# Kernel tuning notes

Hardware: AMD Instinct MI355X
Metric: run time of the kernel (lower is better)

## Reference

```python
import jax, jax.numpy as jnp
import numpy as np

EPS = 1e-8
FS = 10000
WIN_LEN = 256          # N_FRAME
HOP = WIN_LEN // 2     # 128
NFFT = 2 * WIN_LEN     # 512
NUMBAND = 15
MINFREQ = 150
N_INTEL = 30           # N, number of frames per intelligibility segment
BETA = -15.0
DYN_RANGE = 40.0


def _thirdoct(fs, nfft, num_bands, min_freq):
    """One-third octave band matrix (pystoi.utils.thirdoct)."""
    f = np.linspace(0, fs, nfft + 1)[: nfft // 2 + 1]
    k = np.arange(num_bands, dtype=np.float64)
    freq_low = min_freq * np.power(2.0, (2 * k - 1) / 6)
    freq_high = min_freq * np.power(2.0, (2 * k + 1) / 6)
    obm = np.zeros((num_bands, len(f)), dtype=np.float32)
    for i in range(num_bands):
        fl = int(np.argmin(np.square(f - freq_low[i])))
        fh = int(np.argmin(np.square(f - freq_high[i])))
        obm[i, fl:fh] = 1.0
    return obm


def _frame(x, framelen, hop):
    """x: (B, T) -> (B, nf, framelen) sliding frames (static index gather)."""
    T = x.shape[-1]
    nf = (T - framelen) // hop + 1
    idx = np.arange(framelen)[None, :] + hop * np.arange(nf)[:, None]
    return x[:, idx]


def _stoi(est, tgt, win, obm):
    B = tgt.shape[0]
    # ---- VAD: remove silent frames (stable-partition kept frames to front) ----
    xf = _frame(tgt, WIN_LEN, HOP) * win           # (B, nf, L)
    yf = _frame(est, WIN_LEN, HOP) * win
    energies = 20.0 * jnp.log10(jnp.linalg.norm(xf, axis=-1) + EPS)  # (B, nf)
    mask = (energies.max(-1, keepdims=True) - DYN_RANGE - energies) < 0
    nf = xf.shape[1]
    # stable argsort: kept (mask=True -> key 0) frames first, original order preserved
    order = jnp.argsort(jnp.logical_not(mask).astype(jnp.int32), axis=-1)
    xf = jnp.take_along_axis(xf, order[..., None], axis=1)
    yf = jnp.take_along_axis(yf, order[..., None], axis=1)
    counts = mask.sum(-1)                          # (B,) number of kept frames
    keep = (jnp.arange(nf)[None, :] < counts[:, None]).astype(xf.dtype)
    xf = xf * keep[..., None]
    yf = yf * keep[..., None]

    # ---- overlap-and-add (framelen == 2 * hop) -> (B, (nf+1)*HOP) ----
    def ola(fr):
        a = fr[:, :, :HOP].reshape(B, -1)
        b = fr[:, :, HOP:].reshape(B, -1)
        return jnp.pad(a, ((0, 0), (0, HOP))) + jnp.pad(b, ((0, 0), (HOP, 0)))

    x_sil = ola(xf)
    y_sil = ola(yf)

    # mask sorted descending then first element dropped -> ones at positions < count-1
    m = (jnp.arange(nf - 1)[None, :] < (counts[:, None] - 1)).astype(xf.dtype)  # (B, nf-1)

    # ---- STFT via framing + rfft (last frame dropped, as in module) ----
    def stft(x):
        fr = _frame(x, WIN_LEN, HOP)[:, :-1] * win        # (B, nf-1, L)
        return jnp.fft.rfft(fr, n=NFFT, axis=-1)          # (B, nf-1, F)

    x_spec = stft(x_sil) * m[..., None]
    y_spec = stft(y_sil) * m[..., None]

    # ---- one-third octave band energies ----
    x_tob = jnp.sqrt(jnp.einsum('kf,bnf->bkn', obm, jnp.abs(x_spec) ** 2) + EPS)
    y_tob = jnp.sqrt(jnp.einsum('kf,bnf->bkn', obm, jnp.abs(y_spec) ** 2) + EPS)

    # ---- N_INTEL-frame segments (unfold) ----
    n_stft = x_tob.shape[-1]
    M = n_stft - N_INTEL + 1
    sidx = np.arange(N_INTEL)[:, None] + np.arange(M)[None, :]
    x_seg = x_tob[:, :, sidx]                      # (B, K, N, M)
    y_seg = y_tob[:, :, sidx]
    m2 = m[:, N_INTEL - 1:]                        # (B, M)
    x_seg = x_seg * m2[:, None, None, :]
    y_seg = y_seg * m2[:, None, None, :]

    # ---- clipped, normalized correlation (non-extended STOI) ----
    norm_const = jnp.linalg.norm(x_seg, axis=2, keepdims=True) / (
        jnp.linalg.norm(y_seg, axis=2, keepdims=True) + EPS)
    clip_val = 10.0 ** (-BETA / 20.0)
    y_prim = jnp.minimum(y_seg * norm_const, x_seg * (1.0 + clip_val))
    y_prim = y_prim - y_prim.mean(2, keepdims=True)
    x_c = x_seg - x_seg.mean(2, keepdims=True)
    y_prim = y_prim / (jnp.linalg.norm(y_prim, axis=2, keepdims=True) + EPS)
    x_c = x_c / (jnp.linalg.norm(x_c, axis=2, keepdims=True) + EPS)
    corr = (y_prim * x_c).sum(2).mean(1)           # (B, M)
    out = corr.sum(-1) / (m2.sum(-1) + EPS)        # (B,)
    return -out


def setup_inputs() -> dict:
    key = jax.random.key(0)
    k1, k2 = jax.random.split(key)
    B, T = 32, 320000
    targets = jax.random.normal(k1, (B, T), dtype=jnp.float32)
    est_targets = targets + 0.3 * jax.random.normal(k2, (B, T), dtype=jnp.float32)
    win = jnp.asarray(np.hanning(WIN_LEN + 2)[1:-1], dtype=jnp.float32)
    obm = jnp.asarray(_thirdoct(FS, NFFT, NUMBAND, MINFREQ))
    return {"est_targets": est_targets, "targets": targets, "win": win, "obm": obm}


def reference(est_targets, targets, win, obm):
    return _stoi(est_targets, targets, win, obm)
```

## Files before the change

### kernel.cpp

```cpp
#include <hip/hip_runtime.h>
#include <math.h>

#define EPSF 1e-8f
#define WIN_LEN 256
#define HOP 128
#define NBINS 257
#define NUMBAND 15
#define NFRAMES 2499
#define NSTFT 2498
#define N_INTEL 30
#define NSEG 2469
#define NB 32
#define T_LEN 320000
#define CLIP_VAL 5.623413251903491f
#define NHALF 2500
#define AB_STRIDE 2560

typedef float v2f __attribute__((ext_vector_type(2)));
typedef float v4f __attribute__((ext_vector_type(4)));

__device__ __forceinline__ void pk_fma_blo(v2f& d, v2f a, v2f b) {
    asm("v_pk_fma_f32 %0, %1, %2, %0 op_sel:[0,0,0] op_sel_hi:[1,0,1]"
        : "+v"(d) : "v"(a), "v"(b));
}
__device__ __forceinline__ void pk_fma_bhi(v2f& d, v2f a, v2f b) {
    asm("v_pk_fma_f32 %0, %1, %2, %0 op_sel:[0,1,0] op_sel_hi:[1,1,1]"
        : "+v"(d) : "v"(a), "v"(b));
}
__device__ __forceinline__ void pk_fma_rot(v2f& d, v2f a, v2f b) {
    asm("v_pk_fma_f32 %0, %1, %2, %0 op_sel:[1,1,0] op_sel_hi:[0,1,1] neg_lo:[1,0,0]"
        : "+v"(d) : "v"(a), "v"(b));
}
__device__ __forceinline__ void pk_rot(v2f& cs, v2f cksk) {
    v2f t;
    asm("v_pk_mul_f32 %0, %1, %2 op_sel:[0,0] op_sel_hi:[1,0]"
        : "=v"(t) : "v"(cs), "v"(cksk));
    asm("v_pk_fma_f32 %0, %0, %1, %2 op_sel:[1,1,0] op_sel_hi:[0,1,1] neg_lo:[1,0,0]"
        : "+v"(cs) : "v"(cksk), "v"(t));
}
__device__ __forceinline__ v2f pk_cmul(v2f a, v2f b) {
    v2f t;
    asm("v_pk_mul_f32 %0, %1, %2 op_sel:[0,0] op_sel_hi:[1,0]"
        : "=v"(t) : "v"(a), "v"(b));
    asm("v_pk_fma_f32 %0, %1, %2, %0 op_sel:[1,1,0] op_sel_hi:[0,1,1] neg_lo:[1,0,0]"
        : "+v"(t) : "v"(a), "v"(b));
    return t;
}

#define WS_COUNTS   0
#define WS_BANDLO   512
#define WS_BANDHI   768
#define WS_ACC      1024
#define WS_SRCFRM   2048
#define WS_XTOB     324096
#define WS_YTOB     5120512

__global__ __launch_bounds__(256)
void k1a_ab(const float* __restrict__ tgt, const float* __restrict__ win,
            float2* __restrict__ ab)
{
    const int b = blockIdx.x;
    const int h = blockIdx.y * 256 + threadIdx.x;
    if (h >= NHALF) return;
    const float* xp = tgt + (size_t)b * T_LEN + (size_t)h * HOP;
    float sa = 0.f, sb = 0.f;
    #pragma unroll 4
    for (int u = 0; u < HOP; u += 4) {
        const float4 xv = *(const float4*)(xp + u);
        const float4 wl = *(const float4*)(win + u);
        const float4 wh = *(const float4*)(win + HOP + u);
        float a;
        a = xv.x * wl.x; sa = fmaf(a, a, sa);
        a = xv.y * wl.y; sa = fmaf(a, a, sa);
        a = xv.z * wl.z; sa = fmaf(a, a, sa);
        a = xv.w * wl.w; sa = fmaf(a, a, sa);
        a = xv.x * wh.x; sb = fmaf(a, a, sb);
        a = xv.y * wh.y; sb = fmaf(a, a, sb);
        a = xv.z * wh.z; sb = fmaf(a, a, sb);
        a = xv.w * wh.w; sb = fmaf(a, a, sb);
    }
    ab[(size_t)b * AB_STRIDE + h] = make_float2(sa, sb);
}

__global__ __launch_bounds__(256)
void k1b_scan(const float2* __restrict__ ab, const float* __restrict__ obm,
              int* __restrict__ counts, int* __restrict__ srcfrm,
              int* __restrict__ band_lo, int* __restrict__ band_hi,
              float* __restrict__ acc)
{
    const int b = blockIdx.x;
    const int tid = threadIdx.x;
    __shared__ float nr[NFRAMES];
    __shared__ float red[256];
    __shared__ int   sc[256];

    const float2* abp = ab + (size_t)b * AB_STRIDE;
    for (int f = tid; f < NFRAMES; f += 256) {
        const float2 p0 = abp[f];
        const float2 p1 = abp[f + 1];
        nr[f] = sqrtf(p0.x + p1.y);
    }
    __syncthreads();

    float mx = 0.f;
    for (int f = tid; f < NFRAMES; f += 256) mx = fmaxf(mx, nr[f]);
    red[tid] = mx;
    __syncthreads();
    for (int s = 128; s > 0; s >>= 1) {
        if (tid < s) red[tid] = fmaxf(red[tid], red[tid + s]);
        __syncthreads();
    }
    const float thr = (red[0] + EPSF) * 0.01f;

    const int c0 = tid * 10;
    const int c1 = (c0 + 10 < NFRAMES) ? c0 + 10 : NFRAMES;
    int lc = 0;
    for (int f = c0; f < c1; ++f) if (nr[f] + EPSF > thr) ++lc;
    sc[tid] = lc;
    __syncthreads();
    #pragma unroll
    for (int off = 1; off < 256; off <<= 1) {
        int u = (tid >= off) ? sc[tid - off] : 0;
        __syncthreads();
        sc[tid] += u;
        __syncthreads();
    }
    if (tid == 0) {
        counts[b] = sc[255];
        acc[b] = 0.f;
    }
    int pos = sc[tid] - lc;
    int* sf = srcfrm + b * NFRAMES;
    for (int f = c0; f < c1; ++f) if (nr[f] + EPSF > thr) sf[pos++] = f;

    if (b == 0 && tid < NUMBAND) {
        int lo = -1, hi = 0;
        for (int k = 0; k < NBINS; ++k) {
            if (obm[tid * NBINS + k] != 0.f) { if (lo < 0) lo = k; hi = k + 1; }
        }
        band_lo[tid] = (lo < 0) ? 0 : lo;
        band_hi[tid] = hi;
    }
    __syncthreads();
    if (b == 0 && tid == 0) {
        int lo = NBINS, hi = 0;
        for (int i = 0; i < NUMBAND; ++i) {
            if (band_lo[i] < lo) lo = band_lo[i];
            if (band_hi[i] > hi) hi = band_hi[i];
        }
        band_lo[NUMBAND] = lo;
        band_hi[NUMBAND] = hi;
    }
}

__global__ __launch_bounds__(128)
void k2_stft_tob(const float* __restrict__ est, const float* __restrict__ tgt,
                 const float* __restrict__ win,
                 const int* __restrict__ counts, const int* __restrict__ srcfrm,
                 const int* __restrict__ band_lo, const int* __restrict__ band_hi,
                 float* __restrict__ xtob, float* __restrict__ ytob)
{
    const int lin = blockIdx.x;
    const int xcd = lin & 7, cidx = lin >> 3;
    const int q = NSTFT >> 3, r = NSTFT & 7;
    const int j = (xcd < r ? xcd * (q + 1) : r * (q + 1) + (xcd - r) * q) + cidx;

    const int b = blockIdx.y;
    const int cntb = counts[b];
    if (j >= cntb - 1) return;

    const int tid = threadIdx.x;
    __shared__ v4f   sxy[512];
    __shared__ float frf[512];

    const int* sf = srcfrm + b * NFRAMES;
    const float* xg = tgt + (size_t)b * T_LEN;
    const float* yg = est + (size_t)b * T_LEN;

    {
        const int t2 = 2 * tid;
        const int k0 = sf[j];
        const v2f wa = *(const v2f*)&win[t2];
        v2f xv, yv;
        if (tid < 64) {
            xv = *(const v2f*)&xg[k0 * HOP + t2] * wa;
            yv = *(const v2f*)&yg[k0 * HOP + t2] * wa;
            if (j >= 1) {
                const int km = sf[j - 1];
                const v2f wb = *(const v2f*)&win[HOP + t2];
                xv += *(const v2f*)&xg[km * HOP + HOP + t2] * wb;
                yv += *(const v2f*)&yg[km * HOP + HOP + t2] * wb;
            }
        } else {
            const int kp = sf[j + 1];
            const v2f wb = *(const v2f*)&win[t2 - HOP];
            xv = *(const v2f*)&xg[k0 * HOP + t2] * wa
               + *(const v2f*)&xg[kp * HOP + t2 - HOP] * wb;
            yv = *(const v2f*)&yg[k0 * HOP + t2] * wa
               + *(const v2f*)&yg[kp * HOP + t2 - HOP] * wb;
        }
        const v4f st = { xv.x * wa.x, yv.x * wa.x, xv.y * wa.y, yv.y * wa.y };
        *(v4f*)&frf[4 * tid] = st;
    }
    __syncthreads();

    {
        const int m = tid & 7;
        const int c = tid >> 3;
        const float ang = -0.19634954084936207f * (float)m;
        const v2f cksk = { __cosf(ang), __sinf(ang) };
        v2f cs = { 1.f, 0.f };
        v2f Tx0 = {0,0}, Tx1 = {0,0}, Tx2 = {0,0}, Tx3 = {0,0};
        v2f Ty0 = {0,0}, Ty1 = {0,0}, Ty2 = {0,0}, Ty3 = {0,0};
        #pragma unroll
        for (int t1 = 0; t1 < 16; ++t1) {
            const v2f va = *(const v2f*)&frf[2 * (t1 * 16 + c)];
            if ((t1 & 3) == 0)      { pk_fma_blo(Tx0, cs, va); pk_fma_bhi(Ty0, cs, va); }
            else if ((t1 & 3) == 1) { pk_fma_blo(Tx1, cs, va); pk_fma_bhi(Ty1, cs, va); }
            else if ((t1 & 3) == 2) { pk_fma_blo(Tx2, cs, va); pk_fma_bhi(Ty2, cs, va); }
            else                    { pk_fma_blo(Tx3, cs, va); pk_fma_bhi(Ty3, cs, va); }
            pk_rot(cs, cksk);
        }
        const v2f Ax = Tx0 + Tx2, Bx = Tx0 - Tx2, Cx = Tx1 + Tx3, Dx = Tx1 - Tx3;
        const v2f Ay = Ty0 + Ty2, By = Ty0 - Ty2, Cy = Ty1 + Ty3, Dy = Ty1 - Ty3;
        const v2f S0x = Ax + Cx, S2x = Ax - Cx;
        const v2f S0y = Ay + Cy, S2y = Ay - Cy;
        const v2f S1x = { Bx.x + Dx.y, Bx.y - Dx.x };
        const v2f S1y = { By.x + Dy.y, By.y - Dy.x };
        const v2f S3x = { Bx.x - Dx.y, Bx.y + Dx.x };
        const v2f S3y = { By.x - Dy.y, By.y + Dy.x };
        sxy[c * 32 + m]      = (v4f){ S0x.x, S0x.y, S0y.x, S0y.y };
        sxy[c * 32 + m + 8]  = (v4f){ S1x.x, S1x.y, S1y.x, S1y.y };
        sxy[c * 32 + m + 16] = (v4f){ S2x.x, S2x.y, S2y.x, S2y.y };
        sxy[c * 32 + m + 24] = (v4f){ S3x.x, S3x.y, S3y.x, S3y.y };
    }
    __syncthreads();

    const int blo = band_lo[NUMBAND];
    const int bhi = band_hi[NUMBAND];
    (void)bhi;
    const int base = blo & ~31;
    float* px = frf;
    float* py = frf + 224;
    if (tid < 64) {
        const int m2 = tid & 31;
        const int sig = tid >> 5;
        const int sbyte = m2 * 16 + sig * 8;
        const float ang = -0.012271846303085130f * (float)(base + m2);
        const v2f cksk = { __cosf(ang), __sinf(ang) };
        v2f cs = { 1.f, 0.f };
        v2f V[16];
        #pragma unroll
        for (int t0 = 0; t0 < 16; ++t0) {
            const v2f s = *(const v2f*)((const char*)sxy + (t0 * 512 + sbyte));
            V[t0] = (t0 == 0) ? s : pk_cmul(cs, s);
            pk_rot(cs, cksk);
        }
        v2f G[4][4];
        #pragma unroll
        for (int rr = 0; rr < 4; ++rr) {
            const v2f A = V[rr] + V[rr + 8];
            const v2f B = V[rr] - V[rr + 8];
            const v2f C = V[rr + 4] + V[rr + 12];
            const v2f D = V[rr + 4] - V[rr + 12];
            G[0][rr] = A + C;
            G[2][rr] = A - C;
            G[1][rr] = (v2f){ B.x + D.y, B.y - D.x };
            G[3][rr] = (v2f){ B.x - D.y, B.y + D.x };
        }
        float* pout = sig ? py : px;
        #define C1 0.92387953251f
        #define S1 0.38268343236f
        #define C2 0.70710678119f
        #define XOUT(P, D, W1R, W1I, W2R, W2I, W3R, W3I) { \
            float xr_ = G[D][0].x, xi_ = G[D][0].y; \
            xr_ += (W1R)*G[D][1].x - (W1I)*G[D][1].y; xi_ += (W1R)*G[D][1].y + (W1I)*G[D][1].x; \
            xr_ += (W2R)*G[D][2].x - (W2I)*G[D][2].y; xi_ += (W2R)*G[D][2].y + (W2I)*G[D][2].x; \
            xr_ += (W3R)*G[D][3].x - (W3I)*G[D][3].y; xi_ += (W3R)*G[D][3].y + (W3I)*G[D][3].x; \
            pout[(P) * 32 + m2] = fmaf(xr_, xr_, xi_ * xi_); }
        XOUT(0, 0,  1.f, 0.f,    1.f, 0.f,    1.f, 0.f)
        XOUT(1, 1,  C1, -S1,     C2, -C2,     S1, -C1)
        XOUT(2, 2,  C2, -C2,     0.f, -1.f,  -C2, -C2)
        XOUT(3, 3,  S1, -C1,    -C2, -C2,    -C1,  S1)
        XOUT(4, 0,  0.f, -1.f,  -1.f, 0.f,    0.f,  1.f)
        XOUT(5, 1, -S1, -C1,    -C2,  C2,     C1,  S1)
        XOUT(6, 2, -C2, -C2,     0.f,  1.f,   C2, -C2)
        #undef XOUT
    }
    __syncthreads();

    {
        const float* parr = (tid < 64) ? px : py;
        const int lt = (tid < 64) ? tid : tid - 64;
        if (lt < 4 * NUMBAND) {
            const int band = lt >> 2, s = lt & 3;
            const int lop = band_lo[band] - base, hip = band_hi[band] - base;
            const int u0 = lop >> 1, ul = (hip - 1) >> 1;
            float ssum = 0.f;
            for (int u = u0 + s; u <= ul; u += 4) {
                const v2f pv = *(const v2f*)&parr[2 * u];
                ssum += (2 * u >= lop ? pv.x : 0.f) + (2 * u + 1 < hip ? pv.y : 0.f);
            }
            ssum += __shfl_xor(ssum, 1, 64);
            ssum += __shfl_xor(ssum, 2, 64);
            if (s == 0) {
                float* tob = (tid < 64) ? xtob : ytob;
                tob[((size_t)b * NUMBAND + band) * NSTFT + j] = sqrtf(ssum + EPSF);
            }
        }
    }
}

__global__ __launch_bounds__(256)
void k3_corr(const float* __restrict__ xtob, const float* __restrict__ ytob,
             const int* __restrict__ counts, float* __restrict__ acc)
{
    const int bb = blockIdx.y;
    const int b = bb / NUMBAND;
    const int band = bb % NUMBAND;
    const int s_base = blockIdx.x * 256;
    const int tid = threadIdx.x;
    const int seg = s_base + tid;

    __shared__ v2f lxy[256 + N_INTEL - 1];
    const float* xr = xtob + ((size_t)b * NUMBAND + band) * NSTFT;
    const float* yr = ytob + ((size_t)b * NUMBAND + band) * NSTFT;
    for (int i = tid; i < 256 + N_INTEL - 1; i += 256) {
        const int g = s_base + i;
        v2f v = { 0.f, 0.f };
        if (g < NSTFT) v = (v2f){ xr[g], yr[g] };
        lxy[i] = v;
    }
    __syncthreads();

    int nvalid = counts[b] - N_INTEL;
    if (nvalid < 0) nvalid = 0;
    if (nvalid > NSEG) nvalid = NSEG;

    float d = 0.f;
    if (seg < nvalid) {
        float xv[N_INTEL], yv[N_INTEL];
        float sx2 = 0.f, sy2 = 0.f;
        #pragma unroll
        for (int i = 0; i < N_INTEL; ++i) {
            const v2f v = lxy[tid + i];
            xv[i] = v.x; yv[i] = v.y;
            sx2 = fmaf(xv[i], xv[i], sx2);
            sy2 = fmaf(yv[i], yv[i], sy2);
        }
        const float nc = sqrtf(sx2) / (sqrtf(sy2) + EPSF);
        float sy = 0.f, sx = 0.f;
        #pragma unroll
        for (int i = 0; i < N_INTEL; ++i) {
            const float yp = fminf(yv[i] * nc, xv[i] * (1.f + CLIP_VAL));
            yv[i] = yp;
            sy += yp; sx += xv[i];
        }
        const float my = sy * (1.f / N_INTEL);
        const float mxm = sx * (1.f / N_INTEL);
        float num = 0.f, dy = 0.f, dx2 = 0.f;
        #pragma unroll
        for (int i = 0; i < N_INTEL; ++i) {
            const float a = yv[i] - my;
            const float c = xv[i] - mxm;
            num = fmaf(a, c, num);
            dy  = fmaf(a, a, dy);
            dx2 = fmaf(c, c, dx2);
        }
        d = num / ((sqrtf(dy) + EPSF) * (sqrtf(dx2) + EPSF));
    }

    #pragma unroll
    for (int o = 32; o > 0; o >>= 1) d += __shfl_down(d, o, 64);
    __shared__ float wsum[4];
    const int lane = threadIdx.x & 63, wid = threadIdx.x >> 6;
    if (lane == 0) wsum[wid] = d;
    __syncthreads();
    if (threadIdx.x == 0) {
        atomicAdd(&acc[b], wsum[0] + wsum[1] + wsum[2] + wsum[3]);
    }
}

__global__ void k4_final(const float* __restrict__ acc, const int* __restrict__ counts,
                         float* __restrict__ out)
{
    const int b = threadIdx.x;
    if (b < NB) {
        int nvalid = counts[b] - N_INTEL;
        if (nvalid < 0) nvalid = 0;
        if (nvalid > NSEG) nvalid = NSEG;
        out[b] = -(acc[b] * (1.f / NUMBAND)) / ((float)nvalid + EPSF);
    }
}

extern "C" void kernel_launch(void* const* d_in, const int* in_sizes, int n_in,
                              void* d_out, int out_size, void* d_ws, size_t ws_size,
                              hipStream_t stream) {
    (void)in_sizes; (void)n_in; (void)out_size; (void)ws_size;
    const float* est = (const float*)d_in[0];
    const float* tgt = (const float*)d_in[1];
    const float* win = (const float*)d_in[2];
    const float* obm = (const float*)d_in[3];
    float* out = (float*)d_out;

    char* ws = (char*)d_ws;
    int*   counts  = (int*)(ws + WS_COUNTS);
    int*   band_lo = (int*)(ws + WS_BANDLO);
    int*   band_hi = (int*)(ws + WS_BANDHI);
    float* acc     = (float*)(ws + WS_ACC);
    int*   srcfrm  = (int*)(ws + WS_SRCFRM);
    float* xtob    = (float*)(ws + WS_XTOB);
    float* ytob    = (float*)(ws + WS_YTOB);
    float2* ab     = (float2*)xtob;

    k1a_ab<<<dim3(NB, 10), dim3(256), 0, stream>>>(tgt, win, ab);
    k1b_scan<<<dim3(NB), dim3(256), 0, stream>>>(ab, obm, counts, srcfrm,
                                                 band_lo, band_hi, acc);
    k2_stft_tob<<<dim3(NSTFT, NB), dim3(128), 0, stream>>>(est, tgt, win, counts, srcfrm,
                                                           band_lo, band_hi, xtob, ytob);
    k3_corr<<<dim3((NSEG + 255) / 256, NB * NUMBAND), dim3(256), 0, stream>>>(xtob, ytob,
                                                                              counts, acc);
    k4_final<<<1, NB, 0, stream>>>(acc, counts, out);
}
```

Before: 193.7 us.

## Shrink STFT kernel to one wavefront with radix-8 first stage

The STFT/band kernel now runs with 64 threads per block instead of 128. Each thread loads four samples and computes the first FFT stage as a twiddled radix-8 butterfly instead of the old rotating-phasor radix-16 DFT. The intermediate spectrum moves to a padded, planar shared-memory layout, and the final band reduction does both the x and y sums in the same lanes. The aim is to remove idle half-block phases and cut register and LDS traffic. In exchange, each thread does more work, register pressure is higher, and fewer threads are available to hide latency.

```diff
diff --git a/kernel.cpp b/kernel.cpp
--- a/kernel.cpp
+++ b/kernel.cpp
@@ -21,10 +21,6 @@
 
 __device__ __forceinline__ void pk_fma_blo(v2f& d, v2f a, v2f b) {
     asm("v_pk_fma_f32 %0, %1, %2, %0 op_sel:[0,0,0] op_sel_hi:[1,0,1]"
-        : "+v"(d) : "v"(a), "v"(b));
-}
-__device__ __forceinline__ void pk_fma_bhi(v2f& d, v2f a, v2f b) {
-    asm("v_pk_fma_f32 %0, %1, %2, %0 op_sel:[0,1,0] op_sel_hi:[1,1,1]"
         : "+v"(d) : "v"(a), "v"(b));
 }
 __device__ __forceinline__ void pk_fma_rot(v2f& d, v2f a, v2f b) {
@@ -153,7 +149,7 @@
     }
 }
 
-__global__ __launch_bounds__(128)
+__global__ __launch_bounds__(64)
 void k2_stft_tob(const float* __restrict__ est, const float* __restrict__ tgt,
                  const float* __restrict__ win,
                  const int* __restrict__ counts, const int* __restrict__ srcfrm,
@@ -170,89 +166,119 @@
     if (j >= cntb - 1) return;
 
     const int tid = threadIdx.x;
-    __shared__ v4f   sxy[512];
     __shared__ float frf[512];
+    __shared__ float sxr[2 * 16 * 68];
 
     const int* sf = srcfrm + b * NFRAMES;
     const float* xg = tgt + (size_t)b * T_LEN;
     const float* yg = est + (size_t)b * T_LEN;
 
     {
-        const int t2 = 2 * tid;
+        const int t4 = 4 * tid;
         const int k0 = sf[j];
-        const v2f wa = *(const v2f*)&win[t2];
-        v2f xv, yv;
-        if (tid < 64) {
-            xv = *(const v2f*)&xg[k0 * HOP + t2] * wa;
-            yv = *(const v2f*)&yg[k0 * HOP + t2] * wa;
+        const v4f wa = *(const v4f*)&win[t4];
+        v4f xv, yv;
+        if (tid < 32) {
+            xv = *(const v4f*)&xg[k0 * HOP + t4] * wa;
+            yv = *(const v4f*)&yg[k0 * HOP + t4] * wa;
             if (j >= 1) {
                 const int km = sf[j - 1];
-                const v2f wb = *(const v2f*)&win[HOP + t2];
-                xv += *(const v2f*)&xg[km * HOP + HOP + t2] * wb;
-                yv += *(const v2f*)&yg[km * HOP + HOP + t2] * wb;
+                const v4f wb = *(const v4f*)&win[HOP + t4];
+                xv += *(const v4f*)&xg[km * HOP + HOP + t4] * wb;
+                yv += *(const v4f*)&yg[km * HOP + HOP + t4] * wb;
             }
         } else {
             const int kp = sf[j + 1];
-            const v2f wb = *(const v2f*)&win[t2 - HOP];
-            xv = *(const v2f*)&xg[k0 * HOP + t2] * wa
-               + *(const v2f*)&xg[kp * HOP + t2 - HOP] * wb;
-            yv = *(const v2f*)&yg[k0 * HOP + t2] * wa
-               + *(const v2f*)&yg[kp * HOP + t2 - HOP] * wb;
-        }
-        const v4f st = { xv.x * wa.x, yv.x * wa.x, xv.y * wa.y, yv.y * wa.y };
-        *(v4f*)&frf[4 * tid] = st;
+            const v4f wb = *(const v4f*)&win[t4 - HOP];
+            xv = *(const v4f*)&xg[k0 * HOP + t4] * wa
+               + *(const v4f*)&xg[kp * HOP + t4 - HOP] * wb;
+            yv = *(const v4f*)&yg[k0 * HOP + t4] * wa
+               + *(const v4f*)&yg[kp * HOP + t4 - HOP] * wb;
+        }
+        xv *= wa; yv *= wa;
+        const v4f lo = { xv.x, yv.x, xv.y, yv.y };
+        const v4f hi = { xv.z, yv.z, xv.w, yv.w };
+        *(v4f*)&frf[2 * t4]     = lo;
+        *(v4f*)&frf[2 * t4 + 4] = hi;
     }
     __syncthreads();
 
     {
-        const int m = tid & 7;
-        const int c = tid >> 3;
+        const int m = tid & 3;
+        const int c = tid >> 2;
+        const float ke = (m == 0) ? 1.f : (m == 2) ? -1.f : 0.f;
+        const float ki = (m == 1) ? -1.f : (m == 3) ? 1.f : 0.f;
         const float ang = -0.19634954084936207f * (float)m;
-        const v2f cksk = { __cosf(ang), __sinf(ang) };
-        v2f cs = { 1.f, 0.f };
-        v2f Tx0 = {0,0}, Tx1 = {0,0}, Tx2 = {0,0}, Tx3 = {0,0};
-        v2f Ty0 = {0,0}, Ty1 = {0,0}, Ty2 = {0,0}, Ty3 = {0,0};
-        #pragma unroll
-        for (int t1 = 0; t1 < 16; ++t1) {
-            const v2f va = *(const v2f*)&frf[2 * (t1 * 16 + c)];
-            if ((t1 & 3) == 0)      { pk_fma_blo(Tx0, cs, va); pk_fma_bhi(Ty0, cs, va); }
-            else if ((t1 & 3) == 1) { pk_fma_blo(Tx1, cs, va); pk_fma_bhi(Ty1, cs, va); }
-            else if ((t1 & 3) == 2) { pk_fma_blo(Tx2, cs, va); pk_fma_bhi(Ty2, cs, va); }
-            else                    { pk_fma_blo(Tx3, cs, va); pk_fma_bhi(Ty3, cs, va); }
-            pk_rot(cs, cksk);
-        }
-        const v2f Ax = Tx0 + Tx2, Bx = Tx0 - Tx2, Cx = Tx1 + Tx3, Dx = Tx1 - Tx3;
-        const v2f Ay = Ty0 + Ty2, By = Ty0 - Ty2, Cy = Ty1 + Ty3, Dy = Ty1 - Ty3;
-        const v2f S0x = Ax + Cx, S2x = Ax - Cx;
-        const v2f S0y = Ay + Cy, S2y = Ay - Cy;
-        const v2f S1x = { Bx.x + Dx.y, Bx.y - Dx.x };
-        const v2f S1y = { By.x + Dy.y, By.y - Dy.x };
-        const v2f S3x = { Bx.x - Dx.y, Bx.y + Dx.x };
-        const v2f S3y = { By.x - Dy.y, By.y + Dy.x };
-        sxy[c * 32 + m]      = (v4f){ S0x.x, S0x.y, S0y.x, S0y.y };
-        sxy[c * 32 + m + 8]  = (v4f){ S1x.x, S1x.y, S1y.x, S1y.y };
-        sxy[c * 32 + m + 16] = (v4f){ S2x.x, S2x.y, S2y.x, S2y.y };
-        sxy[c * 32 + m + 24] = (v4f){ S3x.x, S3x.y, S3y.x, S3y.y };
+        const float cm0 = __cosf(ang), sm0 = __sinf(ang);
+        v2f URe[8], UIm[8];
+        float cr = 1.f, sr = 0.f;
+        #pragma unroll
+        for (int rr = 0; rr < 8; ++rr) {
+            const v2f za = *(const v2f*)&frf[2 * (16 * rr + c)];
+            const v2f zb = *(const v2f*)&frf[2 * (16 * rr + 128 + c)];
+            const v2f pre_re = za + ke * zb;
+            const v2f pre_im = ki * zb;
+            URe[rr] = cr * pre_re - sr * pre_im;
+            UIm[rr] = sr * pre_re + cr * pre_im;
+            const float crn = cr * cm0 - sr * sm0;
+            sr = sr * cm0 + cr * sm0;
+            cr = crn;
+        }
+        v2f ARe[8], AIm[8];
+        {
+            const float C2 = 0.70710678118654752f;
+            #pragma unroll
+            for (int rr = 0; rr < 4; ++rr) {
+                ARe[rr] = URe[rr] + URe[rr + 4];
+                AIm[rr] = UIm[rr] + UIm[rr + 4];
+            }
+            v2f dR, dI;
+            ARe[4] = URe[0] - URe[4];           AIm[4] = UIm[0] - UIm[4];
+            dR = URe[1] - URe[5]; dI = UIm[1] - UIm[5];
+            ARe[5] = C2 * (dR + dI);            AIm[5] = C2 * (dI - dR);
+            dR = URe[2] - URe[6]; dI = UIm[2] - UIm[6];
+            ARe[6] = dI;                        AIm[6] = -dR;
+            dR = URe[3] - URe[7]; dI = UIm[3] - UIm[7];
+            ARe[7] = C2 * (dI - dR);            AIm[7] = -C2 * (dR + dI);
+        }
+        v2f BRe[8], BIm[8];
+        #pragma unroll
+        for (int g = 0; g < 8; g += 4) {
+            BRe[g + 0] = ARe[g + 0] + ARe[g + 2];  BIm[g + 0] = AIm[g + 0] + AIm[g + 2];
+            BRe[g + 1] = ARe[g + 1] + ARe[g + 3];  BIm[g + 1] = AIm[g + 1] + AIm[g + 3];
+            BRe[g + 2] = ARe[g + 0] - ARe[g + 2];  BIm[g + 2] = AIm[g + 0] - AIm[g + 2];
+            const v2f dR = ARe[g + 1] - ARe[g + 3], dI = AIm[g + 1] - AIm[g + 3];
+            BRe[g + 3] = dI;  BIm[g + 3] = -dR;
+        }
+        const int kmap[8] = { 0, 4, 2, 6, 1, 5, 3, 7 };
+        #pragma unroll
+        for (int p = 0; p < 8; ++p) {
+            const int pb = p & ~1;
+            const float sg = (p & 1) ? -1.f : 1.f;
+            const v2f oR = BRe[pb] + sg * BRe[pb + 1];
+            const v2f oI = BIm[pb] + sg * BIm[pb + 1];
+            const int mj = m + 4 * kmap[p];
+            *(v2f*)&sxr[c * 68 + mj * 2]        = (v2f){ oR.x, oI.x };
+            *(v2f*)&sxr[1088 + c * 68 + mj * 2] = (v2f){ oR.y, oI.y };
+        }
     }
     __syncthreads();
 
     const int blo = band_lo[NUMBAND];
-    const int bhi = band_hi[NUMBAND];
-    (void)bhi;
     const int base = blo & ~31;
     float* px = frf;
     float* py = frf + 224;
-    if (tid < 64) {
+    {
         const int m2 = tid & 31;
         const int sig = tid >> 5;
-        const int sbyte = m2 * 16 + sig * 8;
+        const float* sbase = sxr + sig * 1088 + m2 * 2;
         const float ang = -0.012271846303085130f * (float)(base + m2);
         const v2f cksk = { __cosf(ang), __sinf(ang) };
         v2f cs = { 1.f, 0.f };
         v2f V[16];
         #pragma unroll
         for (int t0 = 0; t0 < 16; ++t0) {
-            const v2f s = *(const v2f*)((const char*)sxy + (t0 * 512 + sbyte));
+            const v2f s = *(const v2f*)(sbase + t0 * 68);
             V[t0] = (t0 == 0) ? s : pk_cmul(cs, s);
             pk_rot(cs, cksk);
         }
@@ -271,7 +297,7 @@
         float* pout = sig ? py : px;
         #define C1 0.92387953251f
         #define S1 0.38268343236f
-        #define C2 0.70710678119f
+        #define C2c 0.70710678119f
         #define XOUT(P, D, W1R, W1I, W2R, W2I, W3R, W3I) { \
             float xr_ = G[D][0].x, xi_ = G[D][0].y; \
             xr_ += (W1R)*G[D][1].x - (W1I)*G[D][1].y; xi_ += (W1R)*G[D][1].y + (W1I)*G[D][1].x; \
@@ -279,34 +305,34 @@
             xr_ += (W3R)*G[D][3].x - (W3I)*G[D][3].y; xi_ += (W3R)*G[D][3].y + (W3I)*G[D][3].x; \
             pout[(P) * 32 + m2] = fmaf(xr_, xr_, xi_ * xi_); }
         XOUT(0, 0,  1.f, 0.f,    1.f, 0.f,    1.f, 0.f)
-        XOUT(1, 1,  C1, -S1,     C2, -C2,     S1, -C1)
-        XOUT(2, 2,  C2, -C2,     0.f, -1.f,  -C2, -C2)
-        XOUT(3, 3,  S1, -C1,    -C2, -C2,    -C1,  S1)
+        XOUT(1, 1,  C1, -S1,     C2c, -C2c,   S1, -C1)
+        XOUT(2, 2,  C2c, -C2c,   0.f, -1.f,  -C2c, -C2c)
+        XOUT(3, 3,  S1, -C1,    -C2c, -C2c,  -C1,  S1)
         XOUT(4, 0,  0.f, -1.f,  -1.f, 0.f,    0.f,  1.f)
-        XOUT(5, 1, -S1, -C1,    -C2,  C2,     C1,  S1)
-        XOUT(6, 2, -C2, -C2,     0.f,  1.f,   C2, -C2)
+        XOUT(5, 1, -S1, -C1,    -C2c,  C2c,   C1,  S1)
+        XOUT(6, 2, -C2c, -C2c,   0.f,  1.f,   C2c, -C2c)
         #undef XOUT
     }
     __syncthreads();
 
-    {
-        const float* parr = (tid < 64) ? px : py;
-        const int lt = (tid < 64) ? tid : tid - 64;
-        if (lt < 4 * NUMBAND) {
-            const int band = lt >> 2, s = lt & 3;
-            const int lop = band_lo[band] - base, hip = band_hi[band] - base;
-            const int u0 = lop >> 1, ul = (hip - 1) >> 1;
-            float ssum = 0.f;
-            for (int u = u0 + s; u <= ul; u += 4) {
-                const v2f pv = *(const v2f*)&parr[2 * u];
-                ssum += (2 * u >= lop ? pv.x : 0.f) + (2 * u + 1 < hip ? pv.y : 0.f);
-            }
-            ssum += __shfl_xor(ssum, 1, 64);
-            ssum += __shfl_xor(ssum, 2, 64);
-            if (s == 0) {
-                float* tob = (tid < 64) ? xtob : ytob;
-                tob[((size_t)b * NUMBAND + band) * NSTFT + j] = sqrtf(ssum + EPSF);
-            }
+    if (tid < 4 * NUMBAND) {
+        const int band = tid >> 2, s = tid & 3;
+        const int lop = band_lo[band] - base, hip = band_hi[band] - base;
+        const int u0 = lop >> 1, ul = (hip - 1) >> 1;
+        float sx = 0.f, sy = 0.f;
+        for (int u = u0 + s; u <= ul; u += 4) {
+            const v2f pvx = *(const v2f*)&px[2 * u];
+            const v2f pvy = *(const v2f*)&py[2 * u];
+            const float m0 = (2 * u >= lop) ? 1.f : 0.f;
+            const float m1 = (2 * u + 1 < hip) ? 1.f : 0.f;
+            sx = fmaf(m0, pvx.x, sx); sx = fmaf(m1, pvx.y, sx);
+            sy = fmaf(m0, pvy.x, sy); sy = fmaf(m1, pvy.y, sy);
+        }
+        sx += __shfl_xor(sx, 1, 64);  sx += __shfl_xor(sx, 2, 64);
+        sy += __shfl_xor(sy, 1, 64);  sy += __shfl_xor(sy, 2, 64);
+        if (s == 0) {
+            xtob[((size_t)b * NUMBAND + band) * NSTFT + j] = sqrtf(sx + EPSF);
+            ytob[((size_t)b * NUMBAND + band) * NSTFT + j] = sqrtf(sy + EPSF);
         }
     }
 }
@@ -416,8 +442,8 @@
     k1a_ab<<<dim3(NB, 10), dim3(256), 0, stream>>>(tgt, win, ab);
     k1b_scan<<<dim3(NB), dim3(256), 0, stream>>>(ab, obm, counts, srcfrm,
                                                  band_lo, band_hi, acc);
-    k2_stft_tob<<<dim3(NSTFT, NB), dim3(128), 0, stream>>>(est, tgt, win, counts, srcfrm,
-                                                           band_lo, band_hi, xtob, ytob);
+    k2_stft_tob<<<dim3(NSTFT, NB), dim3(64), 0, stream>>>(est, tgt, win, counts, srcfrm,
+                                                          band_lo, band_hi, xtob, ytob);
     k3_corr<<<dim3((NSEG + 255) / 256, NB * NUMBAND), dim3(256), 0, stream>>>(xtob, ytob,
                                                                               counts, acc);
     k4_final<<<1, NB, 0, stream>>>(acc, counts, out);
```

New measurement: 191.0 us. No clear change (-1.4%).
